# Performance work log

Hardware: AMD Instinct MI355X
Metric: run time of the kernel (lower is better)

Reference implementation:

```python
import jax, jax.numpy as jnp
import numpy as np

A = 256      # alphabet_size
T = 128      # tag_vector_dim
E = 64       # embedding_dim
H = 64       # hidden_dim (encoder)
NL = 3       # num_layers
B = 4096     # batch
L = 32       # lemma length
STEPS = 30   # decode steps
START = 1    # Alphabet.start_integer (external global in source; fixed here)


def _cell(x, h, c, Wih, Whh, bih, bhh):
    # torch LSTM gate order: i, f, g, o
    g = x @ Wih.T + h @ Whh.T + bih + bhh
    i, f, gg, o = jnp.split(g, 4, axis=-1)
    c = jax.nn.sigmoid(f) * c + jax.nn.sigmoid(i) * jnp.tanh(gg)
    h = jax.nn.sigmoid(o) * jnp.tanh(c)
    return h, c


def _run_layer(xs, Wih, Whh, bih, bhh):
    # xs: [L, B, D] -> ys: [L, B, Hout]; zero initial state (torch default)
    Hout = Whh.shape[1]
    h0 = jnp.zeros((xs.shape[1], Hout), xs.dtype)
    def step(carry, x):
        h, c = _cell(x, carry[0], carry[1], Wih, Whh, bih, bhh)
        return (h, c), h
    _, ys = jax.lax.scan(step, (h0, h0), xs)
    return ys


def setup_inputs() -> dict:
    key = jax.random.key(0)
    ks = jax.random.split(key, 24)
    s = 0.05
    inp = {
        'families': jax.random.randint(ks[0], (B,), 0, 10),
        'languages': jax.random.randint(ks[1], (B,), 0, 20),
        'tags': jax.random.uniform(ks[2], (B, T), dtype=jnp.float32),
        'lemmata': jax.random.randint(ks[3], (B, L), 0, A),
        'emb': jax.random.normal(ks[4], (A, E), jnp.float32) * s,
        # encoder lstm1: layer0 in=T+E, layers 1..2 in=H; hidden=H
        'l1_Wih0': jax.random.normal(ks[5], (4 * H, T + E), jnp.float32) * s,
        'l1_Whh0': jax.random.normal(ks[6], (4 * H, H), jnp.float32) * s,
        'l1_bih0': jnp.zeros((4 * H,), jnp.float32),
        'l1_bhh0': jnp.zeros((4 * H,), jnp.float32),
        'l1_Wih': jax.random.normal(ks[7], (NL - 1, 4 * H, H), jnp.float32) * s,
        'l1_Whh': jax.random.normal(ks[8], (NL - 1, 4 * H, H), jnp.float32) * s,
        'l1_bih': jnp.zeros((NL - 1, 4 * H), jnp.float32),
        'l1_bhh': jnp.zeros((NL - 1, 4 * H), jnp.float32),
        # decoder lstm2: layer0 in=T+A, layers 1..2 in=A; hidden=A
        'l2_Wih0': jax.random.normal(ks[9], (4 * A, T + A), jnp.float32) * s,
        'l2_Whh0': jax.random.normal(ks[10], (4 * A, A), jnp.float32) * s,
        'l2_bih0': jnp.zeros((4 * A,), jnp.float32),
        'l2_bhh0': jnp.zeros((4 * A,), jnp.float32),
        'l2_Wih': jax.random.normal(ks[11], (NL - 1, 4 * A, A), jnp.float32) * s,
        'l2_Whh': jax.random.normal(ks[12], (NL - 1, 4 * A, A), jnp.float32) * s,
        'l2_bih': jnp.zeros((NL - 1, 4 * A), jnp.float32),
        'l2_bhh': jnp.zeros((NL - 1, 4 * A), jnp.float32),
        'lin_W': jax.random.normal(ks[13], (A, A), jnp.float32) * s,
        'lin_b': jnp.zeros((A,), jnp.float32),
    }
    return inp


def reference(families, languages, tags, lemmata, emb,
              l1_Wih0, l1_Whh0, l1_bih0, l1_bhh0, l1_Wih, l1_Whh, l1_bih, l1_bhh,
              l2_Wih0, l2_Whh0, l2_bih0, l2_bhh0, l2_Wih, l2_Whh, l2_bih, l2_bhh,
              lin_W, lin_b):
    tags = tags.astype(jnp.float32)
    # ---- encoder (computed as in source; its output is discarded there too) ----
    x = emb[lemmata]                                   # [B, L, E]
    tags_rep = jnp.broadcast_to(tags[:, None, :], (B, L, T))
    enc_in = jnp.concatenate([x, tags_rep], axis=-1)   # [B, L, E+T]
    ys = jnp.swapaxes(enc_in, 0, 1)                    # [L, B, E+T]
    ys = _run_layer(ys, l1_Wih0, l1_Whh0, l1_bih0, l1_bhh0)
    for k in range(NL - 1):
        ys = _run_layer(ys, l1_Wih[k], l1_Whh[k], l1_bih[k], l1_bhh[k])
    code = ys  # unused downstream, matching original (hidden/cell reset to zero)

    start = jax.nn.one_hot(jnp.full((B,), START), A, dtype=jnp.float32)  # [B, A]
    h0 = jnp.zeros((NL, B, A), jnp.float32)
    c0 = jnp.zeros((NL, B, A), jnp.float32)

    def dstep(carry, _):
        prob, h, c = carry
        xin = jnp.concatenate([prob, tags], axis=-1)   # [B, A+T]
        h0_, c0_ = _cell(xin, h[0], c[0], l2_Wih0, l2_Whh0, l2_bih0, l2_bhh0)
        h1_, c1_ = _cell(h0_, h[1], c[1], l2_Wih[0], l2_Whh[0], l2_bih[0], l2_bhh[0])
        h2_, c2_ = _cell(h1_, h[2], c[2], l2_Wih[1], l2_Whh[1], l2_bih[1], l2_bhh[1])
        pred = jax.nn.sigmoid(h2_ @ lin_W.T + lin_b)   # [B, A]
        new_carry = (pred, jnp.stack([h0_, h1_, h2_]), jnp.stack([c0_, c1_, c2_]))
        return new_carry, (pred, jnp.argmax(pred, axis=-1))

    _, (preds, outs) = jax.lax.scan(dstep, (start, h0, c0), None, length=STEPS)
    probabilities = jnp.concatenate(
        [start[:, None, :], jnp.swapaxes(preds, 0, 1)], axis=1)  # [B, 31, A]
    outputs = jnp.swapaxes(outs, 0, 1)                           # [B, 30]
    return probabilities, outputs
```

## Files before the change

### kernel.cpp

```cpp
#include <hip/hip_runtime.h>
#include <math.h>


typedef float v4 __attribute__((ext_vector_type(4)));
typedef float v2 __attribute__((ext_vector_type(2)));

constexpr int Bsz   = 4096;
constexpr int AA    = 256;
constexpr int STEPS = 30;
constexpr int LDP   = 31 * AA;
constexpr long long PROB_N = (long long)Bsz * 31 * AA;

constexpr int WP0_Q = 160 * 1024;
constexpr int WP1_Q = 128 * 1024;
constexpr int WP2_Q = 128 * 1024;
constexpr int WPL_Q = 64 * 256;
constexpr int WP1_BASE = WP0_Q;
constexpr int WP2_BASE = WP1_BASE + WP1_Q;
constexpr int WPL_BASE = WP2_BASE + WP2_Q;
constexpr int WP_TOTAL = WPL_BASE + WPL_Q;

constexpr int XROWS = 1152;

__device__ __forceinline__ float sigf(float x) { return 1.0f / (1.0f + expf(-x)); }

__global__ void repack_kernel(const float* __restrict__ Wih0, const float* __restrict__ Whh0,
                              const float* __restrict__ Wih12, const float* __restrict__ Whh12,
                              const float* __restrict__ linW, float* __restrict__ ws)
{
    int t = blockIdx.x * 256 + threadIdx.x;
    v4 val;
    if (t < WP1_BASE) {
        int cg = t & 15, j = (t >> 4) & 7, cc = (t >> 7) & 7, q = t >> 10;
        int u = cc * 32 + cg * 2 + (j >> 2);
        int grow = (j & 3) * 256 + u;
        int k4 = q * 4;
        const float* src = (k4 < 384) ? (Wih0 + grow * 384 + k4)
                                      : (Whh0 + grow * 256 + (k4 - 384));
        val = *reinterpret_cast<const v4*>(src);
    } else if (t < WP2_BASE) {
        int tt = t - WP1_BASE;
        int cg = tt & 15, j = (tt >> 4) & 7, cc = (tt >> 7) & 7, q = tt >> 10;
        int u = cc * 32 + cg * 2 + (j >> 2);
        int grow = (j & 3) * 256 + u;
        int k4 = q * 4;
        const float* src = (k4 < 256) ? (Wih12 + grow * 256 + k4)
                                      : (Whh12 + grow * 256 + (k4 - 256));
        val = *reinterpret_cast<const v4*>(src);
    } else if (t < WPL_BASE) {
        int tt = t - WP2_BASE;
        int cg = tt & 15, j = (tt >> 4) & 7, cc = (tt >> 7) & 7, q = tt >> 10;
        int u = cc * 32 + cg * 2 + (j >> 2);
        int grow = (j & 3) * 256 + u;
        int k4 = q * 4;
        const float* src = (k4 < 256) ? (Wih12 + 262144 + grow * 256 + k4)
                                      : (Whh12 + 262144 + grow * 256 + (k4 - 256));
        val = *reinterpret_cast<const v4*>(src);
    } else {
        int tt = t - WPL_BASE;
        int cg = tt & 15, j = (tt >> 4) & 1, cc = (tt >> 5) & 7, q = tt >> 8;
        int n = cc * 32 + cg * 2 + j;
        val = *reinterpret_cast<const v4*>(linW + n * 256 + q * 4);
    }
    reinterpret_cast<v4*>(ws)[t] = val;
}

template<int Q>
__device__ __forceinline__ void lstm_phase(
    const v4* __restrict__ wq, const float* __restrict__ xb,
    const float* __restrict__ bihL, const float* __restrict__ bhhL,
    int u0, int rg, float (&cr)[2][4], float* __restrict__ dst)
{
    float bs[8];
    #pragma unroll
    for (int j = 0; j < 8; j++) {
        int grow = (j & 3) * 256 + u0 + (j >> 2);
        bs[j] = bihL[grow] + bhhL[grow];
    }
    float acc[8][4];
    #pragma unroll
    for (int j = 0; j < 8; j++)
        #pragma unroll
        for (int r = 0; r < 4; r++) acc[j][r] = 0.0f;

    const v4* xq = reinterpret_cast<const v4*>(xb) + rg;
    v4 wa[8], wb[8], xa[4], xc[4];

    #pragma unroll
    for (int j = 0; j < 8; j++) wa[j] = wq[j * 16];
    #pragma unroll
    for (int k = 0; k < 4; k++) xa[k] = xq[k * 4];

    #pragma unroll 1
    for (int q = 0; q < Q - 2; q += 2) {
        #pragma unroll
        for (int j = 0; j < 8; j++) wb[j] = wq[(q + 1) * 1024 + j * 16];
        #pragma unroll
        for (int k = 0; k < 4; k++) xc[k] = xq[((q + 1) * 4 + k) * 4];
        #pragma unroll
        for (int k = 0; k < 4; k++)
            #pragma unroll
            for (int j = 0; j < 8; j++)
                #pragma unroll
                for (int r = 0; r < 4; r++)
                    acc[j][r] += wa[j][k] * xa[k][r];
        #pragma unroll
        for (int j = 0; j < 8; j++) wa[j] = wq[(q + 2) * 1024 + j * 16];
        #pragma unroll
        for (int k = 0; k < 4; k++) xa[k] = xq[((q + 2) * 4 + k) * 4];
        #pragma unroll
        for (int k = 0; k < 4; k++)
            #pragma unroll
            for (int j = 0; j < 8; j++)
                #pragma unroll
                for (int r = 0; r < 4; r++)
                    acc[j][r] += wb[j][k] * xc[k][r];
    }
    #pragma unroll
    for (int j = 0; j < 8; j++) wb[j] = wq[(Q - 1) * 1024 + j * 16];
    #pragma unroll
    for (int k = 0; k < 4; k++) xc[k] = xq[((Q - 1) * 4 + k) * 4];
    #pragma unroll
    for (int k = 0; k < 4; k++)
        #pragma unroll
        for (int j = 0; j < 8; j++)
            #pragma unroll
            for (int r = 0; r < 4; r++)
                acc[j][r] += wa[j][k] * xa[k][r];
    #pragma unroll
    for (int k = 0; k < 4; k++)
        #pragma unroll
        for (int j = 0; j < 8; j++)
            #pragma unroll
            for (int r = 0; r < 4; r++)
                acc[j][r] += wb[j][k] * xc[k][r];

    __syncthreads();
    #pragma unroll
    for (int ul = 0; ul < 2; ul++) {
        int u = u0 + ul;
        v4 hv;
        #pragma unroll
        for (int r = 0; r < 4; r++) {
            float gi = acc[ul * 4 + 0][r] + bs[ul * 4 + 0];
            float gf = acc[ul * 4 + 1][r] + bs[ul * 4 + 1];
            float gg = acc[ul * 4 + 2][r] + bs[ul * 4 + 2];
            float go = acc[ul * 4 + 3][r] + bs[ul * 4 + 3];
            float cn = sigf(gf) * cr[ul][r] + sigf(gi) * tanhf(gg);
            cr[ul][r] = cn;
            hv[r] = sigf(go) * tanhf(cn);
        }
        *reinterpret_cast<v4*>(dst + u * 16 + rg * 4) = hv;
    }
    __syncthreads();
}

__device__ __forceinline__ void lin_phase(
    const v4* __restrict__ wq, const float* __restrict__ xb,
    const float* __restrict__ linb,
    int u0, int rg, int m0, int t,
    float* __restrict__ probdst, float* __restrict__ out)
{
    float bs[2] = { linb[u0], linb[u0 + 1] };
    float acc[2][4];
    #pragma unroll
    for (int j = 0; j < 2; j++)
        #pragma unroll
        for (int r = 0; r < 4; r++) acc[j][r] = 0.0f;

    const v4* xq = reinterpret_cast<const v4*>(xb) + rg;
    v4 wa[2], wb[2], xa[4], xc[4];
    #pragma unroll
    for (int j = 0; j < 2; j++) wa[j] = wq[j * 16];
    #pragma unroll
    for (int k = 0; k < 4; k++) xa[k] = xq[k * 4];

    #pragma unroll 1
    for (int q = 0; q < 62; q += 2) {
        #pragma unroll
        for (int j = 0; j < 2; j++) wb[j] = wq[(q + 1) * 256 + j * 16];
        #pragma unroll
        for (int k = 0; k < 4; k++) xc[k] = xq[((q + 1) * 4 + k) * 4];
        #pragma unroll
        for (int k = 0; k < 4; k++)
            #pragma unroll
            for (int j = 0; j < 2; j++)
                #pragma unroll
                for (int r = 0; r < 4; r++)
                    acc[j][r] += wa[j][k] * xa[k][r];
        #pragma unroll
        for (int j = 0; j < 2; j++) wa[j] = wq[(q + 2) * 256 + j * 16];
        #pragma unroll
        for (int k = 0; k < 4; k++) xa[k] = xq[((q + 2) * 4 + k) * 4];
        #pragma unroll
        for (int k = 0; k < 4; k++)
            #pragma unroll
            for (int j = 0; j < 2; j++)
                #pragma unroll
                for (int r = 0; r < 4; r++)
                    acc[j][r] += wb[j][k] * xc[k][r];
    }
    #pragma unroll
    for (int j = 0; j < 2; j++) wb[j] = wq[63 * 256 + j * 16];
    #pragma unroll
    for (int k = 0; k < 4; k++) xc[k] = xq[(63 * 4 + k) * 4];
    #pragma unroll
    for (int k = 0; k < 4; k++)
        #pragma unroll
        for (int j = 0; j < 2; j++)
            #pragma unroll
            for (int r = 0; r < 4; r++)
                acc[j][r] += wa[j][k] * xa[k][r];
    #pragma unroll
    for (int k = 0; k < 4; k++)
        #pragma unroll
        for (int j = 0; j < 2; j++)
            #pragma unroll
            for (int r = 0; r < 4; r++)
                acc[j][r] += wb[j][k] * xc[k][r];

    __syncthreads();
    v4 pv[2];
    #pragma unroll
    for (int j = 0; j < 2; j++) {
        #pragma unroll
        for (int r = 0; r < 4; r++) pv[j][r] = sigf(acc[j][r] + bs[j]);
        *reinterpret_cast<v4*>(probdst + (u0 + j) * 16 + rg * 4) = pv[j];
    }
    #pragma unroll
    for (int r = 0; r < 4; r++) {
        v2 f2; f2[0] = pv[0][r]; f2[1] = pv[1][r];
        *reinterpret_cast<v2*>(out + (long long)(m0 + rg * 4 + r) * LDP
                                   + (long long)(t + 1) * AA + u0) = f2;
    }
    __syncthreads();
}

__global__ __launch_bounds__(512) void decode_kernel(
    const float* __restrict__ tags,
    const float* __restrict__ bih0, const float* __restrict__ bhh0,
    const float* __restrict__ bih12, const float* __restrict__ bhh12,
    const float* __restrict__ linb,
    const float* __restrict__ ws,
    float* __restrict__ out)
{
    __shared__ float X[XROWS * 16];
    __shared__ float redv[512];
    __shared__ int   redi[512];

    const int tid  = threadIdx.x;
    const int c    = tid >> 6;
    const int lane = tid & 63;
    const int cg   = lane & 15;
    const int rg   = lane >> 4;
    const int u0   = c * 32 + cg * 2;
    const int m0   = blockIdx.x * 16;

    for (int i = tid; i < XROWS * 16; i += 512) X[i] = 0.0f;
    __syncthreads();
    for (int i = tid; i < 128 * 16; i += 512) {
        int m = i & 15, k = i >> 4;
        X[(256 + k) * 16 + m] = tags[(long long)(m0 + m) * 128 + k];
    }
    if (tid < 16) X[1 * 16 + tid] = 1.0f;
    for (int i = tid; i < 256 * 16; i += 512) {
        int m = i >> 8, col = i & 255;
        out[(long long)(m0 + m) * LDP + col] = (col == 1) ? 1.0f : 0.0f;
    }
    __syncthreads();

    float cr0[2][4], cr1[2][4], cr2[2][4];
    #pragma unroll
    for (int a = 0; a < 2; a++)
        #pragma unroll
        for (int b = 0; b < 4; b++) { cr0[a][b] = 0.f; cr1[a][b] = 0.f; cr2[a][b] = 0.f; }

    const v4* wsq = reinterpret_cast<const v4*>(ws);
    const v4* w0 = wsq + 0        + c * 128 + cg;
    const v4* w1 = wsq + WP1_BASE + c * 128 + cg;
    const v4* w2 = wsq + WP2_BASE + c * 128 + cg;
    const v4* wl = wsq + WPL_BASE + c * 32  + cg;

    float* hx0 = X + 384 * 16;
    float* hx1 = X + 640 * 16;
    float* hx2 = X + 896 * 16;

    const int arow = tid & 15, sb = tid >> 4;
    float* outputs = out + PROB_N;

    #pragma unroll 1
    for (int t = 0; t < STEPS; t++) {
        lstm_phase<160>(w0, X,   bih0,        bhh0,        u0, rg, cr0, hx0);
        lstm_phase<128>(w1, hx0, bih12,       bhh12,       u0, rg, cr1, hx1);
        lstm_phase<128>(w2, hx1, bih12+1024,  bhh12+1024,  u0, rg, cr2, hx2);
        lin_phase(wl, hx2, linb, u0, rg, m0, t, X, out);

        float bv = -1.0f; int bi = 0;
        #pragma unroll
        for (int i = 0; i < 8; i++) {
            int u = sb * 8 + i;
            float v = X[u * 16 + arow];
            if (v > bv) { bv = v; bi = u; }
        }
        redv[sb * 16 + arow] = bv;
        redi[sb * 16 + arow] = bi;
        __syncthreads();
        if (tid < 16) {
            float v0 = redv[tid]; int i0 = redi[tid];
            #pragma unroll 1
            for (int s = 1; s < 32; s++) {
                float v = redv[s * 16 + tid]; int ii = redi[s * 16 + tid];
                if (v > v0 || (v == v0 && ii < i0)) { v0 = v; i0 = ii; }
            }
            outputs[(long long)(m0 + tid) * STEPS + t] = (float)i0;
        }
    }
}

extern "C" void kernel_launch(void* const* d_in, const int* in_sizes, int n_in,
                              void* d_out, int out_size, void* d_ws, size_t ws_size,
                              hipStream_t stream) {
    const float* tags  = (const float*)d_in[2];
    const float* Wih0  = (const float*)d_in[13];
    const float* Whh0  = (const float*)d_in[14];
    const float* bih0  = (const float*)d_in[15];
    const float* bhh0  = (const float*)d_in[16];
    const float* Wih12 = (const float*)d_in[17];
    const float* Whh12 = (const float*)d_in[18];
    const float* bih12 = (const float*)d_in[19];
    const float* bhh12 = (const float*)d_in[20];
    const float* linW  = (const float*)d_in[21];
    const float* linb  = (const float*)d_in[22];

    float* out = (float*)d_out;
    float* ws  = (float*)d_ws;

    repack_kernel<<<WP_TOTAL / 256, 256, 0, stream>>>(Wih0, Whh0, Wih12, Whh12,
                                                      linW, ws);
    decode_kernel<<<Bsz / 16, 512, 0, stream>>>(
        tags, bih0, bhh0, bih12, bhh12, linb, ws, out);
}
```

Measured before the change: 7.377 ms.

## Double decoder block threads to 1024, one hidden unit per thread

Each block now runs 1024 threads instead of 512, so each thread owns one hidden unit (four gate rows) rather than two, halving per-thread accumulators and weight registers. The weight repack layout, the linear-layer mapping and the argmax reduction are reworked to match the new thread-to-unit mapping. The aim is more waves per block to hide global weight-load latency in the per-step LSTM GEMVs. In exchange, more threads take part in each barrier, the final argmax scan is longer, and the tighter register budget may cause spills.

```diff
diff --git a/kernel.cpp b/kernel.cpp
--- a/kernel.cpp
+++ b/kernel.cpp
@@ -3,7 +3,6 @@
 
 
 typedef float v4 __attribute__((ext_vector_type(4)));
-typedef float v2 __attribute__((ext_vector_type(2)));
 
 constexpr int Bsz   = 4096;
 constexpr int AA    = 256;
@@ -31,212 +30,167 @@
     int t = blockIdx.x * 256 + threadIdx.x;
     v4 val;
     if (t < WP1_BASE) {
-        int cg = t & 15, j = (t >> 4) & 7, cc = (t >> 7) & 7, q = t >> 10;
-        int u = cc * 32 + cg * 2 + (j >> 2);
-        int grow = (j & 3) * 256 + u;
+        int cg = t & 15, j = (t >> 4) & 3, c = (t >> 6) & 15, q = t >> 10;
+        int grow = j * 256 + c * 16 + cg;
         int k4 = q * 4;
         const float* src = (k4 < 384) ? (Wih0 + grow * 384 + k4)
                                       : (Whh0 + grow * 256 + (k4 - 384));
         val = *reinterpret_cast<const v4*>(src);
     } else if (t < WP2_BASE) {
         int tt = t - WP1_BASE;
-        int cg = tt & 15, j = (tt >> 4) & 7, cc = (tt >> 7) & 7, q = tt >> 10;
-        int u = cc * 32 + cg * 2 + (j >> 2);
-        int grow = (j & 3) * 256 + u;
+        int cg = tt & 15, j = (tt >> 4) & 3, c = (tt >> 6) & 15, q = tt >> 10;
+        int grow = j * 256 + c * 16 + cg;
         int k4 = q * 4;
         const float* src = (k4 < 256) ? (Wih12 + grow * 256 + k4)
                                       : (Whh12 + grow * 256 + (k4 - 256));
         val = *reinterpret_cast<const v4*>(src);
     } else if (t < WPL_BASE) {
         int tt = t - WP2_BASE;
-        int cg = tt & 15, j = (tt >> 4) & 7, cc = (tt >> 7) & 7, q = tt >> 10;
-        int u = cc * 32 + cg * 2 + (j >> 2);
-        int grow = (j & 3) * 256 + u;
+        int cg = tt & 15, j = (tt >> 4) & 3, c = (tt >> 6) & 15, q = tt >> 10;
+        int grow = j * 256 + c * 16 + cg;
         int k4 = q * 4;
         const float* src = (k4 < 256) ? (Wih12 + 262144 + grow * 256 + k4)
                                       : (Whh12 + 262144 + grow * 256 + (k4 - 256));
         val = *reinterpret_cast<const v4*>(src);
     } else {
         int tt = t - WPL_BASE;
-        int cg = tt & 15, j = (tt >> 4) & 1, cc = (tt >> 5) & 7, q = tt >> 8;
-        int n = cc * 32 + cg * 2 + j;
+        int cg = tt & 15, c = (tt >> 4) & 15, q = tt >> 8;
+        int n = c * 16 + cg;
         val = *reinterpret_cast<const v4*>(linW + n * 256 + q * 4);
     }
     reinterpret_cast<v4*>(ws)[t] = val;
 }
+
+#define FMA_BLOCK(W, Xv)                                   \
+    _Pragma("unroll")                                      \
+    for (int k = 0; k < 4; k++)                            \
+        _Pragma("unroll")                                  \
+        for (int j = 0; j < 4; j++)                        \
+            _Pragma("unroll")                              \
+            for (int r = 0; r < 4; r++)                    \
+                acc[j][r] += W[j][k] * Xv[k][r];
 
 template<int Q>
 __device__ __forceinline__ void lstm_phase(
     const v4* __restrict__ wq, const float* __restrict__ xb,
     const float* __restrict__ bihL, const float* __restrict__ bhhL,
-    int u0, int rg, float (&cr)[2][4], float* __restrict__ dst)
-{
-    float bs[8];
-    #pragma unroll
-    for (int j = 0; j < 8; j++) {
-        int grow = (j & 3) * 256 + u0 + (j >> 2);
-        bs[j] = bihL[grow] + bhhL[grow];
-    }
-    float acc[8][4];
-    #pragma unroll
-    for (int j = 0; j < 8; j++)
+    int u, int rg, float (&cr)[4], float* __restrict__ dst)
+{
+    float bs[4];
+    #pragma unroll
+    for (int j = 0; j < 4; j++) bs[j] = bihL[j * 256 + u] + bhhL[j * 256 + u];
+
+    float acc[4][4];
+    #pragma unroll
+    for (int j = 0; j < 4; j++)
         #pragma unroll
         for (int r = 0; r < 4; r++) acc[j][r] = 0.0f;
 
     const v4* xq = reinterpret_cast<const v4*>(xb) + rg;
-    v4 wa[8], wb[8], xa[4], xc[4];
-
-    #pragma unroll
-    for (int j = 0; j < 8; j++) wa[j] = wq[j * 16];
+    const v4* wp = wq;
+    v4 wa[4], wb[4], xa[4], xc[4];
+
+    #pragma unroll
+    for (int j = 0; j < 4; j++) wa[j] = wp[j * 16];
+    wp += 1024;
     #pragma unroll
     for (int k = 0; k < 4; k++) xa[k] = xq[k * 4];
 
     #pragma unroll 1
     for (int q = 0; q < Q - 2; q += 2) {
         #pragma unroll
-        for (int j = 0; j < 8; j++) wb[j] = wq[(q + 1) * 1024 + j * 16];
-        #pragma unroll
-        for (int k = 0; k < 4; k++) xc[k] = xq[((q + 1) * 4 + k) * 4];
-        #pragma unroll
-        for (int k = 0; k < 4; k++)
-            #pragma unroll
-            for (int j = 0; j < 8; j++)
-                #pragma unroll
-                for (int r = 0; r < 4; r++)
-                    acc[j][r] += wa[j][k] * xa[k][r];
-        #pragma unroll
-        for (int j = 0; j < 8; j++) wa[j] = wq[(q + 2) * 1024 + j * 16];
-        #pragma unroll
-        for (int k = 0; k < 4; k++) xa[k] = xq[((q + 2) * 4 + k) * 4];
-        #pragma unroll
-        for (int k = 0; k < 4; k++)
-            #pragma unroll
-            for (int j = 0; j < 8; j++)
-                #pragma unroll
-                for (int r = 0; r < 4; r++)
-                    acc[j][r] += wb[j][k] * xc[k][r];
-    }
-    #pragma unroll
-    for (int j = 0; j < 8; j++) wb[j] = wq[(Q - 1) * 1024 + j * 16];
-    #pragma unroll
-    for (int k = 0; k < 4; k++) xc[k] = xq[((Q - 1) * 4 + k) * 4];
-    #pragma unroll
-    for (int k = 0; k < 4; k++)
-        #pragma unroll
-        for (int j = 0; j < 8; j++)
-            #pragma unroll
-            for (int r = 0; r < 4; r++)
-                acc[j][r] += wa[j][k] * xa[k][r];
-    #pragma unroll
-    for (int k = 0; k < 4; k++)
-        #pragma unroll
-        for (int j = 0; j < 8; j++)
-            #pragma unroll
-            for (int r = 0; r < 4; r++)
-                acc[j][r] += wb[j][k] * xc[k][r];
-
-    __syncthreads();
-    #pragma unroll
-    for (int ul = 0; ul < 2; ul++) {
-        int u = u0 + ul;
-        v4 hv;
-        #pragma unroll
-        for (int r = 0; r < 4; r++) {
-            float gi = acc[ul * 4 + 0][r] + bs[ul * 4 + 0];
-            float gf = acc[ul * 4 + 1][r] + bs[ul * 4 + 1];
-            float gg = acc[ul * 4 + 2][r] + bs[ul * 4 + 2];
-            float go = acc[ul * 4 + 3][r] + bs[ul * 4 + 3];
-            float cn = sigf(gf) * cr[ul][r] + sigf(gi) * tanhf(gg);
-            cr[ul][r] = cn;
-            hv[r] = sigf(go) * tanhf(cn);
-        }
-        *reinterpret_cast<v4*>(dst + u * 16 + rg * 4) = hv;
-    }
+        for (int j = 0; j < 4; j++) wb[j] = wp[j * 16];
+        wp += 1024;
+        #pragma unroll
+        for (int k = 0; k < 4; k++) xc[k] = xq[(q + 1) * 16 + k * 4];
+        FMA_BLOCK(wa, xa)
+        #pragma unroll
+        for (int j = 0; j < 4; j++) wa[j] = wp[j * 16];
+        wp += 1024;
+        #pragma unroll
+        for (int k = 0; k < 4; k++) xa[k] = xq[(q + 2) * 16 + k * 4];
+        FMA_BLOCK(wb, xc)
+    }
+    #pragma unroll
+    for (int j = 0; j < 4; j++) wb[j] = wp[j * 16];
+    #pragma unroll
+    for (int k = 0; k < 4; k++) xc[k] = xq[(Q - 1) * 16 + k * 4];
+    FMA_BLOCK(wa, xa)
+    FMA_BLOCK(wb, xc)
+
+    __syncthreads();
+    v4 hv;
+    #pragma unroll
+    for (int r = 0; r < 4; r++) {
+        float gi = acc[0][r] + bs[0];
+        float gf = acc[1][r] + bs[1];
+        float gg = acc[2][r] + bs[2];
+        float go = acc[3][r] + bs[3];
+        float cn = sigf(gf) * cr[r] + sigf(gi) * tanhf(gg);
+        cr[r] = cn;
+        hv[r] = sigf(go) * tanhf(cn);
+    }
+    *reinterpret_cast<v4*>(dst + u * 16 + rg * 4) = hv;
     __syncthreads();
 }
 
 __device__ __forceinline__ void lin_phase(
     const v4* __restrict__ wq, const float* __restrict__ xb,
     const float* __restrict__ linb,
-    int u0, int rg, int m0, int t,
+    int n, int rg, int m0, int t,
     float* __restrict__ probdst, float* __restrict__ out)
 {
-    float bs[2] = { linb[u0], linb[u0 + 1] };
-    float acc[2][4];
-    #pragma unroll
-    for (int j = 0; j < 2; j++)
-        #pragma unroll
-        for (int r = 0; r < 4; r++) acc[j][r] = 0.0f;
-
+    float b = linb[n];
+    float acc[4] = {0.f, 0.f, 0.f, 0.f};
     const v4* xq = reinterpret_cast<const v4*>(xb) + rg;
-    v4 wa[2], wb[2], xa[4], xc[4];
-    #pragma unroll
-    for (int j = 0; j < 2; j++) wa[j] = wq[j * 16];
+    const v4* wp = wq;
+    v4 wa, wb, xa[4], xc[4];
+
+    wa = wp[0]; wp += 256;
     #pragma unroll
     for (int k = 0; k < 4; k++) xa[k] = xq[k * 4];
 
     #pragma unroll 1
     for (int q = 0; q < 62; q += 2) {
-        #pragma unroll
-        for (int j = 0; j < 2; j++) wb[j] = wq[(q + 1) * 256 + j * 16];
-        #pragma unroll
-        for (int k = 0; k < 4; k++) xc[k] = xq[((q + 1) * 4 + k) * 4];
+        wb = wp[0]; wp += 256;
+        #pragma unroll
+        for (int k = 0; k < 4; k++) xc[k] = xq[(q + 1) * 16 + k * 4];
         #pragma unroll
         for (int k = 0; k < 4; k++)
             #pragma unroll
-            for (int j = 0; j < 2; j++)
-                #pragma unroll
-                for (int r = 0; r < 4; r++)
-                    acc[j][r] += wa[j][k] * xa[k][r];
-        #pragma unroll
-        for (int j = 0; j < 2; j++) wa[j] = wq[(q + 2) * 256 + j * 16];
-        #pragma unroll
-        for (int k = 0; k < 4; k++) xa[k] = xq[((q + 2) * 4 + k) * 4];
+            for (int r = 0; r < 4; r++) acc[r] += wa[k] * xa[k][r];
+        wa = wp[0]; wp += 256;
+        #pragma unroll
+        for (int k = 0; k < 4; k++) xa[k] = xq[(q + 2) * 16 + k * 4];
         #pragma unroll
         for (int k = 0; k < 4; k++)
             #pragma unroll
-            for (int j = 0; j < 2; j++)
-                #pragma unroll
-                for (int r = 0; r < 4; r++)
-                    acc[j][r] += wb[j][k] * xc[k][r];
-    }
-    #pragma unroll
-    for (int j = 0; j < 2; j++) wb[j] = wq[63 * 256 + j * 16];
-    #pragma unroll
-    for (int k = 0; k < 4; k++) xc[k] = xq[(63 * 4 + k) * 4];
+            for (int r = 0; r < 4; r++) acc[r] += wb[k] * xc[k][r];
+    }
+    wb = wp[0];
+    #pragma unroll
+    for (int k = 0; k < 4; k++) xc[k] = xq[63 * 16 + k * 4];
     #pragma unroll
     for (int k = 0; k < 4; k++)
         #pragma unroll
-        for (int j = 0; j < 2; j++)
-            #pragma unroll
-            for (int r = 0; r < 4; r++)
-                acc[j][r] += wa[j][k] * xa[k][r];
+        for (int r = 0; r < 4; r++) acc[r] += wa[k] * xa[k][r];
     #pragma unroll
     for (int k = 0; k < 4; k++)
         #pragma unroll
-        for (int j = 0; j < 2; j++)
-            #pragma unroll
-            for (int r = 0; r < 4; r++)
-                acc[j][r] += wb[j][k] * xc[k][r];
-
-    __syncthreads();
-    v4 pv[2];
-    #pragma unroll
-    for (int j = 0; j < 2; j++) {
-        #pragma unroll
-        for (int r = 0; r < 4; r++) pv[j][r] = sigf(acc[j][r] + bs[j]);
-        *reinterpret_cast<v4*>(probdst + (u0 + j) * 16 + rg * 4) = pv[j];
-    }
-    #pragma unroll
-    for (int r = 0; r < 4; r++) {
-        v2 f2; f2[0] = pv[0][r]; f2[1] = pv[1][r];
-        *reinterpret_cast<v2*>(out + (long long)(m0 + rg * 4 + r) * LDP
-                                   + (long long)(t + 1) * AA + u0) = f2;
-    }
-    __syncthreads();
-}
-
-__global__ __launch_bounds__(512) void decode_kernel(
+        for (int r = 0; r < 4; r++) acc[r] += wb[k] * xc[k][r];
+
+    __syncthreads();
+    v4 pv;
+    #pragma unroll
+    for (int r = 0; r < 4; r++) pv[r] = sigf(acc[r] + b);
+    *reinterpret_cast<v4*>(probdst + n * 16 + rg * 4) = pv;
+    #pragma unroll
+    for (int r = 0; r < 4; r++)
+        out[(long long)(m0 + rg * 4 + r) * LDP + (long long)(t + 1) * AA + n] = pv[r];
+    __syncthreads();
+}
+
+__global__ __launch_bounds__(1024) void decode_kernel(
     const float* __restrict__ tags,
     const float* __restrict__ bih0, const float* __restrict__ bhh0,
     const float* __restrict__ bih12, const float* __restrict__ bhh12,
@@ -245,41 +199,39 @@
     float* __restrict__ out)
 {
     __shared__ float X[XROWS * 16];
-    __shared__ float redv[512];
-    __shared__ int   redi[512];
+    __shared__ float redv[1024];
+    __shared__ int   redi[1024];
 
     const int tid  = threadIdx.x;
     const int c    = tid >> 6;
     const int lane = tid & 63;
     const int cg   = lane & 15;
     const int rg   = lane >> 4;
-    const int u0   = c * 32 + cg * 2;
+    const int u    = c * 16 + cg;
     const int m0   = blockIdx.x * 16;
 
-    for (int i = tid; i < XROWS * 16; i += 512) X[i] = 0.0f;
-    __syncthreads();
-    for (int i = tid; i < 128 * 16; i += 512) {
+    for (int i = tid; i < XROWS * 16; i += 1024) X[i] = 0.0f;
+    __syncthreads();
+    for (int i = tid; i < 128 * 16; i += 1024) {
         int m = i & 15, k = i >> 4;
         X[(256 + k) * 16 + m] = tags[(long long)(m0 + m) * 128 + k];
     }
     if (tid < 16) X[1 * 16 + tid] = 1.0f;
-    for (int i = tid; i < 256 * 16; i += 512) {
+    for (int i = tid; i < 256 * 16; i += 1024) {
         int m = i >> 8, col = i & 255;
         out[(long long)(m0 + m) * LDP + col] = (col == 1) ? 1.0f : 0.0f;
     }
     __syncthreads();
 
-    float cr0[2][4], cr1[2][4], cr2[2][4];
-    #pragma unroll
-    for (int a = 0; a < 2; a++)
-        #pragma unroll
-        for (int b = 0; b < 4; b++) { cr0[a][b] = 0.f; cr1[a][b] = 0.f; cr2[a][b] = 0.f; }
+    float cr0[4], cr1[4], cr2[4];
+    #pragma unroll
+    for (int r = 0; r < 4; r++) { cr0[r] = 0.f; cr1[r] = 0.f; cr2[r] = 0.f; }
 
     const v4* wsq = reinterpret_cast<const v4*>(ws);
-    const v4* w0 = wsq + 0        + c * 128 + cg;
-    const v4* w1 = wsq + WP1_BASE + c * 128 + cg;
-    const v4* w2 = wsq + WP2_BASE + c * 128 + cg;
-    const v4* wl = wsq + WPL_BASE + c * 32  + cg;
+    const v4* w0 = wsq + 0        + c * 64 + cg;
+    const v4* w1 = wsq + WP1_BASE + c * 64 + cg;
+    const v4* w2 = wsq + WP2_BASE + c * 64 + cg;
+    const v4* wl = wsq + WPL_BASE + c * 16 + cg;
 
     float* hx0 = X + 384 * 16;
     float* hx1 = X + 640 * 16;
@@ -290,17 +242,17 @@
 
     #pragma unroll 1
     for (int t = 0; t < STEPS; t++) {
-        lstm_phase<160>(w0, X,   bih0,        bhh0,        u0, rg, cr0, hx0);
-        lstm_phase<128>(w1, hx0, bih12,       bhh12,       u0, rg, cr1, hx1);
-        lstm_phase<128>(w2, hx1, bih12+1024,  bhh12+1024,  u0, rg, cr2, hx2);
-        lin_phase(wl, hx2, linb, u0, rg, m0, t, X, out);
+        lstm_phase<160>(w0, X,   bih0,         bhh0,         u, rg, cr0, hx0);
+        lstm_phase<128>(w1, hx0, bih12,        bhh12,        u, rg, cr1, hx1);
+        lstm_phase<128>(w2, hx1, bih12 + 1024, bhh12 + 1024, u, rg, cr2, hx2);
+        lin_phase(wl, hx2, linb, u, rg, m0, t, X, out);
 
         float bv = -1.0f; int bi = 0;
         #pragma unroll
-        for (int i = 0; i < 8; i++) {
-            int u = sb * 8 + i;
-            float v = X[u * 16 + arow];
-            if (v > bv) { bv = v; bi = u; }
+        for (int i = 0; i < 4; i++) {
+            int uu = sb * 4 + i;
+            float v = X[uu * 16 + arow];
+            if (v > bv) { bv = v; bi = uu; }
         }
         redv[sb * 16 + arow] = bv;
         redi[sb * 16 + arow] = bi;
@@ -308,7 +260,7 @@
         if (tid < 16) {
             float v0 = redv[tid]; int i0 = redi[tid];
             #pragma unroll 1
-            for (int s = 1; s < 32; s++) {
+            for (int s = 1; s < 64; s++) {
                 float v = redv[s * 16 + tid]; int ii = redi[s * 16 + tid];
                 if (v > v0 || (v == v0 && ii < i0)) { v0 = v; i0 = ii; }
             }
@@ -337,6 +289,6 @@
 
     repack_kernel<<<WP_TOTAL / 256, 256, 0, stream>>>(Wih0, Whh0, Wih12, Whh12,
                                                       linW, ws);
-    decode_kernel<<<Bsz / 16, 512, 0, stream>>>(
+    decode_kernel<<<Bsz / 16, 1024, 0, stream>>>(
         tags, bih0, bhh0, bih12, bhh12, linb, ws, out);
 }
```

After: 7.964 ms. 8.0% more time.
